# Kernel optimization log

Hardware: AMD Instinct MI355X
Metric: run time of the kernel (lower is better)

## Reference

```python
import jax, jax.numpy as jnp
import numpy as np

N_M = 100000   # metric nodes
N_A = 20000    # alert nodes
E_C = 1600000  # metric->metric 'correlation' edges
E_K = 800000   # metric->alert 'cause' edges
F_IN = 64      # raw feature dim (lazy in_channels in PyG)
DIMS = [128, 256]  # out_dim // 2**(num_layers-i-1) for lstm_dim=256, num_layers=2
NEG_SLOPE = 0.01   # nn.LeakyReLU default


def _lin(key, fan_in, fan_out):
    s = 1.0 / np.sqrt(fan_in)
    return jax.random.uniform(key, (fan_in, fan_out), minval=-s, maxval=s, dtype=jnp.float32)


def setup_inputs() -> dict:
    key = jax.random.key(0)
    ks = jax.random.split(key, 32)
    inp = {
        'x_metric': jax.random.normal(ks[0], (N_M, F_IN), dtype=jnp.float32),
        'x_alert': jax.random.normal(ks[1], (N_A, F_IN), dtype=jnp.float32),
        'w_corr': jax.random.uniform(ks[2], (E_C,), dtype=jnp.float32),
        'w_cause': jax.random.uniform(ks[3], (E_K,), dtype=jnp.float32),
        'src_corr': jax.random.randint(ks[4], (E_C,), 0, N_M, dtype=jnp.int32),
        'dst_corr': jax.random.randint(ks[5], (E_C,), 0, N_M, dtype=jnp.int32),
        'src_cause': jax.random.randint(ks[6], (E_K,), 0, N_M, dtype=jnp.int32),
        'dst_cause': jax.random.randint(ks[7], (E_K,), 0, N_A, dtype=jnp.int32),
    }
    # GraphConv params: lin_rel (with bias) applied to aggregated messages,
    # lin_root (no bias) applied to destination features. Two convs per layer.
    kidx = 8
    in_m, in_a = F_IN, F_IN
    for li, d in enumerate(DIMS):
        inp[f'Wr_c{li}'] = _lin(ks[kidx], in_m, d); kidx += 1  # corr rel
        inp[f'br_c{li}'] = jnp.zeros((d,), jnp.float32)
        inp[f'Wo_c{li}'] = _lin(ks[kidx], in_m, d); kidx += 1  # corr root (dst=metric)
        inp[f'Wr_k{li}'] = _lin(ks[kidx], in_m, d); kidx += 1  # cause rel (src=metric)
        inp[f'br_k{li}'] = jnp.zeros((d,), jnp.float32)
        inp[f'Wo_k{li}'] = _lin(ks[kidx], in_a, d); kidx += 1  # cause root (dst=alert)
        in_m, in_a = d, d
    return inp


def _leaky(x):
    return jnp.where(x > 0, x, NEG_SLOPE * x)


def reference(x_metric, x_alert, w_corr, w_cause,
              src_corr, dst_corr, src_cause, dst_cause,
              Wr_c0, br_c0, Wo_c0, Wr_k0, br_k0, Wo_k0,
              Wr_c1, br_c1, Wo_c1, Wr_k1, br_k1, Wo_k1):
    xm, xa = x_metric, x_alert
    layers = [(Wr_c0, br_c0, Wo_c0, Wr_k0, br_k0, Wo_k0),
              (Wr_c1, br_c1, Wo_c1, Wr_k1, br_k1, Wo_k1)]
    for Wrc, brc, Woc, Wrk, brk, Wok in layers:
        # metric <- metric, GraphConv aggr='add'
        msg_c = xm[src_corr] * w_corr[:, None]                 # [E_C, d_in]
        agg_c = jax.ops.segment_sum(msg_c, dst_corr, num_segments=N_M)
        new_m = agg_c @ Wrc + brc + xm @ Woc
        # alert <- metric, GraphConv aggr='max' (empty segments -> 0, torch_scatter convention)
        msg_k = xm[src_cause] * w_cause[:, None]               # [E_K, d_in]
        agg_k = jax.ops.segment_max(msg_k, dst_cause, num_segments=N_A)
        agg_k = jnp.where(jnp.isfinite(agg_k), agg_k, 0.0)
        new_a = agg_k @ Wrk + brk + xa @ Wok
        xm = _leaky(new_m)
        xa = _leaky(new_a)
    return xa  # HGNN.forward returns x['alert']
```

## Files before the change

### kernel.cpp

```cpp
#include <hip/hip_runtime.h>

#define N_M 100000
#define N_A 20000
#define E_C 1600000
#define E_K 800000
#define CH 2048
#define NXCD 8


__global__ __launch_bounds__(256) void hist_part(const int* __restrict__ dst,
                                                 int* __restrict__ deg,
                                                 int nE, int nodes_per_part) {
    int chunk = blockIdx.x >> 3, part = blockIdx.x & 7;
    int lo = part * nodes_per_part, hi = lo + nodes_per_part;
    int base = chunk * CH + threadIdx.x;
    #pragma unroll
    for (int k = 0; k < 8; ++k) {
        int e = base + k * 256;
        if (e < nE) {
            int d = dst[e];
            if (d >= lo && d < hi) atomicAdd(&deg[d], 1);
        }
    }
}

__global__ __launch_bounds__(256) void fill_eids_part(const int* __restrict__ dst,
                                                      int* __restrict__ cursor,
                                                      int* __restrict__ eids,
                                                      int nE, int nodes_per_part) {
    int chunk = blockIdx.x >> 3, part = blockIdx.x & 7;
    int lo = part * nodes_per_part, hi = lo + nodes_per_part;
    int base = chunk * CH + threadIdx.x;
    #pragma unroll
    for (int k = 0; k < 8; ++k) {
        int e = base + k * 256;
        if (e < nE) {
            int d = dst[e];
            if (d >= lo && d < hi) {
                int p = atomicAdd(&cursor[d], 1);
                eids[p] = e;
            }
        }
    }
}

__global__ __launch_bounds__(256) void fill_pay_part(const int* __restrict__ dst,
                                                     const int* __restrict__ src,
                                                     const float* __restrict__ w,
                                                     int* __restrict__ cursor,
                                                     int* __restrict__ csr_src,
                                                     float* __restrict__ csr_w,
                                                     int nE, int nodes_per_part) {
    int chunk = blockIdx.x >> 3, part = blockIdx.x & 7;
    int lo = part * nodes_per_part, hi = lo + nodes_per_part;
    int base = chunk * CH + threadIdx.x;
    #pragma unroll
    for (int k = 0; k < 8; ++k) {
        int e = base + k * 256;
        if (e < nE) {
            int d = dst[e];
            if (d >= lo && d < hi) {
                int p = atomicAdd(&cursor[d], 1);
                csr_src[p] = src[e];
                csr_w[p]   = w[e];
            }
        }
    }
}


__global__ __launch_bounds__(256) void scan_p1(const int* __restrict__ deg,
                                               int* __restrict__ partial, int n) {
    __shared__ int red[256];
    int base = blockIdx.x * CH + threadIdx.x;
    int s = 0;
    #pragma unroll
    for (int k = 0; k < 8; ++k) { int i = base + k * 256; if (i < n) s += deg[i]; }
    red[threadIdx.x] = s; __syncthreads();
    for (int off = 128; off > 0; off >>= 1) {
        if (threadIdx.x < off) red[threadIdx.x] += red[threadIdx.x + off];
        __syncthreads();
    }
    if (threadIdx.x == 0) partial[blockIdx.x] = red[0];
}

__global__ __launch_bounds__(64) void scan_p2(int* __restrict__ partial,
                                              int* __restrict__ rowptr_end, int P) {
    int lane = threadIdx.x;
    int v = (lane < P) ? partial[lane] : 0;
    int incl = v;
    for (int off = 1; off < 64; off <<= 1) {
        int t = __shfl_up(incl, off);
        if (lane >= off) incl += t;
    }
    if (lane < P) partial[lane] = incl - v;
    if (lane == 63) *rowptr_end = incl;
}

__global__ __launch_bounds__(256) void scan_p3(const int* __restrict__ deg,
                                               const int* __restrict__ partial,
                                               int* __restrict__ rowptr,
                                               int* __restrict__ cursor, int n) {
    __shared__ int buf[256];
    int base = blockIdx.x * CH;
    int v[8]; int lsum = 0;
    #pragma unroll
    for (int k = 0; k < 8; ++k) {
        int i = base + threadIdx.x * 8 + k;
        v[k] = (i < n) ? deg[i] : 0; lsum += v[k];
    }
    buf[threadIdx.x] = lsum; __syncthreads();
    for (int off = 1; off < 256; off <<= 1) {
        int t = (threadIdx.x >= off) ? buf[threadIdx.x - off] : 0;
        __syncthreads(); buf[threadIdx.x] += t; __syncthreads();
    }
    int excl = buf[threadIdx.x] - lsum + partial[blockIdx.x];
    #pragma unroll
    for (int k = 0; k < 8; ++k) {
        int i = base + threadIdx.x * 8 + k;
        if (i < n) { rowptr[i] = excl; cursor[i] = excl; }
        excl += v[k];
    }
}


__global__ __launch_bounds__(256) void agg_sum_d64(
    const float* __restrict__ x, const float* __restrict__ w, const int* __restrict__ src,
    const int* __restrict__ rowptr, const int* __restrict__ eids,
    float* __restrict__ out, int n) {
    int gw = blockIdx.x * 4 + (threadIdx.x >> 6);
    int lane = threadIdx.x & 63;
    if (gw >= n) return;
    int j = rowptr[gw], end = rowptr[gw + 1];
    float acc = 0.f;
    for (; j + 4 <= end; j += 4) {
        int e0 = eids[j], e1 = eids[j + 1], e2 = eids[j + 2], e3 = eids[j + 3];
        int s0 = src[e0], s1 = src[e1], s2 = src[e2], s3 = src[e3];
        float w0 = w[e0], w1 = w[e1], w2 = w[e2], w3 = w[e3];
        float v0 = x[(size_t)s0 * 64 + lane];
        float v1 = x[(size_t)s1 * 64 + lane];
        float v2 = x[(size_t)s2 * 64 + lane];
        float v3 = x[(size_t)s3 * 64 + lane];
        acc = fmaf(v0, w0, acc); acc = fmaf(v1, w1, acc);
        acc = fmaf(v2, w2, acc); acc = fmaf(v3, w3, acc);
    }
    for (; j < end; ++j) {
        int e = eids[j];
        acc = fmaf(x[(size_t)src[e] * 64 + lane], w[e], acc);
    }
    out[(size_t)gw * 64 + lane] = acc;
}

__global__ __launch_bounds__(256) void agg_max_d64_p(
    const float* __restrict__ x, const int* __restrict__ csr_src,
    const float* __restrict__ csr_w, const int* __restrict__ rowptr,
    float* __restrict__ out, int n) {
    int gw = blockIdx.x * 4 + (threadIdx.x >> 6);
    int lane = threadIdx.x & 63;
    if (gw >= n) return;
    int beg = rowptr[gw], end = rowptr[gw + 1];
    float acc = -INFINITY;
    int j = beg;
    for (; j + 4 <= end; j += 4) {
        int s0 = csr_src[j], s1 = csr_src[j + 1], s2 = csr_src[j + 2], s3 = csr_src[j + 3];
        float w0 = csr_w[j], w1 = csr_w[j + 1], w2 = csr_w[j + 2], w3 = csr_w[j + 3];
        float v0 = x[(size_t)s0 * 64 + lane];
        float v1 = x[(size_t)s1 * 64 + lane];
        float v2 = x[(size_t)s2 * 64 + lane];
        float v3 = x[(size_t)s3 * 64 + lane];
        acc = fmaxf(acc, v0 * w0); acc = fmaxf(acc, v1 * w1);
        acc = fmaxf(acc, v2 * w2); acc = fmaxf(acc, v3 * w3);
    }
    for (; j < end; ++j)
        acc = fmaxf(acc, x[(size_t)csr_src[j] * 64 + lane] * csr_w[j]);
    if (beg == end) acc = 0.f;
    out[(size_t)gw * 64 + lane] = acc;
}

__global__ __launch_bounds__(256) void agg_max_d128_p(
    const float* __restrict__ x, const int* __restrict__ csr_src,
    const float* __restrict__ csr_w, const int* __restrict__ rowptr,
    float* __restrict__ out, int n) {
    int gw = blockIdx.x * 4 + (threadIdx.x >> 6);
    int lane = threadIdx.x & 63;
    if (gw >= n) return;
    int beg = rowptr[gw], end = rowptr[gw + 1];
    float ax = -INFINITY, ay = -INFINITY;
    int j = beg;
    for (; j + 2 <= end; j += 2) {
        int s0 = csr_src[j], s1 = csr_src[j + 1];
        float w0 = csr_w[j], w1 = csr_w[j + 1];
        float2 v0 = ((const float2*)(x + (size_t)s0 * 128))[lane];
        float2 v1 = ((const float2*)(x + (size_t)s1 * 128))[lane];
        ax = fmaxf(ax, v0.x * w0); ay = fmaxf(ay, v0.y * w0);
        ax = fmaxf(ax, v1.x * w1); ay = fmaxf(ay, v1.y * w1);
    }
    for (; j < end; ++j) {
        float ww = csr_w[j];
        float2 v = ((const float2*)(x + (size_t)csr_src[j] * 128))[lane];
        ax = fmaxf(ax, v.x * ww); ay = fmaxf(ay, v.y * ww);
    }
    if (beg == end) { ax = 0.f; ay = 0.f; }
    ((float2*)(out + (size_t)gw * 128))[lane] = make_float2(ax, ay);
}

__global__ __launch_bounds__(256) void dual_gemm_leaky(
    const float* __restrict__ A1, const float* __restrict__ A2,
    const float* __restrict__ W1, const float* __restrict__ W2,
    const float* __restrict__ bias, float* __restrict__ out,
    int M, int N, int K1, int K2) {
    constexpr int BM = 64, BN = 64, BK = 16;
    __shared__ float sA[BK][BM];
    __shared__ float sB[BK][BN];
    const int tid = threadIdx.x;
    const int bm0 = blockIdx.y * BM;
    const int bn0 = blockIdx.x * BN;
    const int K = K1 + K2;
    float acc[4][4] = {};
    const int ty = tid >> 4, tx = tid & 15;

    for (int k0 = 0; k0 < K; k0 += BK) {
        #pragma unroll
        for (int i = 0; i < (BM * BK) / 256; ++i) {
            int idx = tid + i * 256;
            int m = idx & (BM - 1);
            int k = idx >> 6;
            int gm = bm0 + m, gk = k0 + k;
            float v = 0.0f;
            if (gm < M)
                v = (gk < K1) ? A1[(size_t)gm * K1 + gk]
                              : A2[(size_t)gm * K2 + (gk - K1)];
            sA[k][m] = v;
        }
        #pragma unroll
        for (int i = 0; i < (BK * BN) / 256; ++i) {
            int idx = tid + i * 256;
            int n = idx & (BN - 1);
            int k = idx >> 6;
            int gk = k0 + k;
            float v = (gk < K1) ? W1[(size_t)gk * N + bn0 + n]
                                : W2[(size_t)(gk - K1) * N + bn0 + n];
            sB[k][n] = v;
        }
        __syncthreads();
        #pragma unroll
        for (int kk = 0; kk < BK; ++kk) {
            float a[4], b[4];
            #pragma unroll
            for (int i = 0; i < 4; ++i) a[i] = sA[kk][ty * 4 + i];
            #pragma unroll
            for (int j = 0; j < 4; ++j) b[j] = sB[kk][tx * 4 + j];
            #pragma unroll
            for (int i = 0; i < 4; ++i)
                #pragma unroll
                for (int j = 0; j < 4; ++j)
                    acc[i][j] = fmaf(a[i], b[j], acc[i][j]);
        }
        __syncthreads();
    }
    #pragma unroll
    for (int i = 0; i < 4; ++i) {
        int gm = bm0 + ty * 4 + i;
        if (gm >= M) continue;
        #pragma unroll
        for (int j = 0; j < 4; ++j) {
            int gn = bn0 + tx * 4 + j;
            float v = acc[i][j] + bias[gn];
            out[(size_t)gm * N + gn] = (v > 0.0f) ? v : 0.01f * v;
        }
    }
}

extern "C" void kernel_launch(void* const* d_in, const int* in_sizes, int n_in,
                              void* d_out, int out_size, void* d_ws, size_t ws_size,
                              hipStream_t stream) {
    const float* x_metric = (const float*)d_in[0];
    const float* x_alert  = (const float*)d_in[1];
    const float* w_corr   = (const float*)d_in[2];
    const float* w_cause  = (const float*)d_in[3];
    const int* src_corr   = (const int*)d_in[4];
    const int* dst_corr   = (const int*)d_in[5];
    const int* src_cause  = (const int*)d_in[6];
    const int* dst_cause  = (const int*)d_in[7];
    const float* Wr_c0 = (const float*)d_in[8];
    const float* br_c0 = (const float*)d_in[9];
    const float* Wo_c0 = (const float*)d_in[10];
    const float* Wr_k0 = (const float*)d_in[11];
    const float* br_k0 = (const float*)d_in[12];
    const float* Wo_k0 = (const float*)d_in[13];
    const float* Wr_k1 = (const float*)d_in[17];
    const float* br_k1 = (const float*)d_in[18];
    const float* Wo_k1 = (const float*)d_in[19];

    float* ws = (float*)d_ws;
    float* xm0   = ws;
    float* aggk0 = ws + 11520000;
    int*   corr_rowptr = (int*)(ws + 12800000);
    int*   corr_eids   = (int*)(ws + 12900016);
    float* xa0         = ws + 12800000;
    int*   cause_rowptr = (int*)(ws + 15360000);
    int*   cause_src    = (int*)(ws + 15380016);
    float* cause_w      = ws + 16180016;
    int*   corr_cursor  = (int*)(ws + 16980016);
    int*   cause_cursor = (int*)(ws + 17080016);
    int*   corr_part    = (int*)(ws + 17100016);
    int*   cause_part   = (int*)(ws + 17100080);
    float* aggm  = ws + 17100160;
    float* aggk1 = ws + 17100160;

    const int corr_chunks  = (E_C + CH - 1) / CH;
    const int cause_chunks = (E_K + CH - 1) / CH;
    const int corr_P  = (N_M + CH - 1) / CH;
    const int cause_P = (N_A + CH - 1) / CH;

    hipMemsetAsync(corr_cursor, 0, (size_t)(N_M + N_A) * 4, stream);
    hist_part<<<corr_chunks * NXCD, 256, 0, stream>>>(dst_corr, corr_cursor, E_C, N_M / NXCD);
    hist_part<<<cause_chunks * NXCD, 256, 0, stream>>>(dst_cause, cause_cursor, E_K, N_A / NXCD);
    scan_p1<<<corr_P, 256, 0, stream>>>(corr_cursor, corr_part, N_M);
    scan_p1<<<cause_P, 256, 0, stream>>>(cause_cursor, cause_part, N_A);
    scan_p2<<<1, 64, 0, stream>>>(corr_part, corr_rowptr + N_M, corr_P);
    scan_p2<<<1, 64, 0, stream>>>(cause_part, cause_rowptr + N_A, cause_P);
    scan_p3<<<corr_P, 256, 0, stream>>>(corr_cursor, corr_part, corr_rowptr, corr_cursor, N_M);
    scan_p3<<<cause_P, 256, 0, stream>>>(cause_cursor, cause_part, cause_rowptr, cause_cursor, N_A);
    fill_eids_part<<<corr_chunks * NXCD, 256, 0, stream>>>(dst_corr, corr_cursor, corr_eids, E_C, N_M / NXCD);
    fill_pay_part<<<cause_chunks * NXCD, 256, 0, stream>>>(dst_cause, src_cause, w_cause,
                                                           cause_cursor, cause_src, cause_w,
                                                           E_K, N_A / NXCD);

    agg_sum_d64<<<(N_M + 3) / 4, 256, 0, stream>>>(x_metric, w_corr, src_corr,
                                                   corr_rowptr, corr_eids, aggm, N_M);
    agg_max_d64_p<<<(N_A + 3) / 4, 256, 0, stream>>>(x_metric, cause_src, cause_w,
                                                     cause_rowptr, aggk0, N_A);

    {
        dim3 grid(128 / 64, (N_A + 63) / 64);
        dual_gemm_leaky<<<grid, 256, 0, stream>>>(aggk0, x_alert, Wr_k0, Wo_k0, br_k0,
                                                  xa0, N_A, 128, 64, 64);
    }
    {
        dim3 grid(128 / 64, (N_M + 63) / 64);
        dual_gemm_leaky<<<grid, 256, 0, stream>>>(aggm, x_metric, Wr_c0, Wo_c0, br_c0,
                                                  xm0, N_M, 128, 64, 64);
    }

    agg_max_d128_p<<<(N_A + 3) / 4, 256, 0, stream>>>(xm0, cause_src, cause_w,
                                                      cause_rowptr, aggk1, N_A);
    {
        dim3 grid(256 / 64, (N_A + 63) / 64);
        dual_gemm_leaky<<<grid, 256, 0, stream>>>(aggk1, xa0, Wr_k1, Wo_k1, br_k1,
                                                  (float*)d_out, N_A, 256, 128, 128);
    }
}
```

Before: 719.2 us.

## Convert features and weights to bf16 and use MFMA dual GEMMs

Casts node features and weights to bf16 and stores intermediate aggregates and activations as bf16, which halves gather traffic in the aggregation kernels. The scalar FP32 dual GEMM is replaced by a templated kernel built on bf16 MFMA 16x16x32 instructions. The correlation CSR now holds src and weight payloads directly instead of edge ids, removing one level of indirection. The cost is reduced precision, which risks accuracy tolerance, plus three extra cast kernels.

```diff
diff --git a/kernel.cpp b/kernel.cpp
--- a/kernel.cpp
+++ b/kernel.cpp
@@ -7,6 +7,44 @@
 #define CH 2048
 #define NXCD 8
 
+typedef __attribute__((ext_vector_type(8)))  short  short8_t;
+typedef __attribute__((ext_vector_type(8)))  unsigned short ushort8_t;
+typedef __attribute__((ext_vector_type(4)))  unsigned short ushort4_t;
+typedef __attribute__((ext_vector_type(4)))  float  f32x4;
+
+__device__ __forceinline__ unsigned short f2b(float f) {
+    unsigned u = __float_as_uint(f);
+    return (unsigned short)((u + 0x7fffu + ((u >> 16) & 1u)) >> 16);
+}
+__device__ __forceinline__ float b2f(unsigned short h) {
+    return __uint_as_float((unsigned)h << 16);
+}
+
+__global__ __launch_bounds__(256) void cast_f32_bf16(const float* __restrict__ in,
+                                                     unsigned short* __restrict__ out, int n) {
+    int i = (blockIdx.x * 256 + threadIdx.x) * 4;
+    if (i >= n) return;
+    float4 v = *(const float4*)(in + i);
+    ushort4_t o; o.x = f2b(v.x); o.y = f2b(v.y); o.z = f2b(v.z); o.w = f2b(v.w);
+    *(ushort4_t*)(out + i) = o;
+}
+
+__global__ __launch_bounds__(256) void cast_weights(
+    const float* rc0, const float* oc0, const float* rk0, const float* ok0,
+    const float* rk1, const float* ok1, unsigned short* __restrict__ wb) {
+    int i = (blockIdx.x * 256 + threadIdx.x) * 4;
+    if (i >= 98304) return;
+    const float* src; int off;
+    if      (i < 8192)  { src = rc0; off = 0; }
+    else if (i < 16384) { src = oc0; off = 8192; }
+    else if (i < 24576) { src = rk0; off = 16384; }
+    else if (i < 32768) { src = ok0; off = 24576; }
+    else if (i < 65536) { src = rk1; off = 32768; }
+    else                { src = ok1; off = 65536; }
+    float4 v = *(const float4*)(src + (i - off));
+    ushort4_t o; o.x = f2b(v.x); o.y = f2b(v.y); o.z = f2b(v.z); o.w = f2b(v.w);
+    *(ushort4_t*)(wb + i) = o;
+}
 
 __global__ __launch_bounds__(256) void hist_part(const int* __restrict__ dst,
                                                  int* __restrict__ deg,
@@ -20,26 +58,6 @@
         if (e < nE) {
             int d = dst[e];
             if (d >= lo && d < hi) atomicAdd(&deg[d], 1);
-        }
-    }
-}
-
-__global__ __launch_bounds__(256) void fill_eids_part(const int* __restrict__ dst,
-                                                      int* __restrict__ cursor,
-                                                      int* __restrict__ eids,
-                                                      int nE, int nodes_per_part) {
-    int chunk = blockIdx.x >> 3, part = blockIdx.x & 7;
-    int lo = part * nodes_per_part, hi = lo + nodes_per_part;
-    int base = chunk * CH + threadIdx.x;
-    #pragma unroll
-    for (int k = 0; k < 8; ++k) {
-        int e = base + k * 256;
-        if (e < nE) {
-            int d = dst[e];
-            if (d >= lo && d < hi) {
-                int p = atomicAdd(&cursor[d], 1);
-                eids[p] = e;
-            }
         }
     }
 }
@@ -68,7 +86,6 @@
     }
 }
 
-
 __global__ __launch_bounds__(256) void scan_p1(const int* __restrict__ deg,
                                                int* __restrict__ partial, int n) {
     __shared__ int red[256];
@@ -123,38 +140,34 @@
     }
 }
 
-
-__global__ __launch_bounds__(256) void agg_sum_d64(
-    const float* __restrict__ x, const float* __restrict__ w, const int* __restrict__ src,
-    const int* __restrict__ rowptr, const int* __restrict__ eids,
-    float* __restrict__ out, int n) {
+__global__ __launch_bounds__(256) void agg_sum_d64_b(
+    const unsigned short* __restrict__ x, const int* __restrict__ csr_src,
+    const float* __restrict__ csr_w, const int* __restrict__ rowptr,
+    unsigned short* __restrict__ out, int n) {
     int gw = blockIdx.x * 4 + (threadIdx.x >> 6);
     int lane = threadIdx.x & 63;
     if (gw >= n) return;
     int j = rowptr[gw], end = rowptr[gw + 1];
     float acc = 0.f;
     for (; j + 4 <= end; j += 4) {
-        int e0 = eids[j], e1 = eids[j + 1], e2 = eids[j + 2], e3 = eids[j + 3];
-        int s0 = src[e0], s1 = src[e1], s2 = src[e2], s3 = src[e3];
-        float w0 = w[e0], w1 = w[e1], w2 = w[e2], w3 = w[e3];
-        float v0 = x[(size_t)s0 * 64 + lane];
-        float v1 = x[(size_t)s1 * 64 + lane];
-        float v2 = x[(size_t)s2 * 64 + lane];
-        float v3 = x[(size_t)s3 * 64 + lane];
+        int s0 = csr_src[j], s1 = csr_src[j+1], s2 = csr_src[j+2], s3 = csr_src[j+3];
+        float w0 = csr_w[j], w1 = csr_w[j+1], w2 = csr_w[j+2], w3 = csr_w[j+3];
+        float v0 = b2f(x[(size_t)s0 * 64 + lane]);
+        float v1 = b2f(x[(size_t)s1 * 64 + lane]);
+        float v2 = b2f(x[(size_t)s2 * 64 + lane]);
+        float v3 = b2f(x[(size_t)s3 * 64 + lane]);
         acc = fmaf(v0, w0, acc); acc = fmaf(v1, w1, acc);
         acc = fmaf(v2, w2, acc); acc = fmaf(v3, w3, acc);
     }
-    for (; j < end; ++j) {
-        int e = eids[j];
-        acc = fmaf(x[(size_t)src[e] * 64 + lane], w[e], acc);
-    }
-    out[(size_t)gw * 64 + lane] = acc;
-}
-
-__global__ __launch_bounds__(256) void agg_max_d64_p(
-    const float* __restrict__ x, const int* __restrict__ csr_src,
+    for (; j < end; ++j)
+        acc = fmaf(b2f(x[(size_t)csr_src[j] * 64 + lane]), csr_w[j], acc);
+    out[(size_t)gw * 64 + lane] = f2b(acc);
+}
+
+__global__ __launch_bounds__(256) void agg_max_d64_b(
+    const unsigned short* __restrict__ x, const int* __restrict__ csr_src,
     const float* __restrict__ csr_w, const int* __restrict__ rowptr,
-    float* __restrict__ out, int n) {
+    unsigned short* __restrict__ out, int n) {
     int gw = blockIdx.x * 4 + (threadIdx.x >> 6);
     int lane = threadIdx.x & 63;
     if (gw >= n) return;
@@ -162,25 +175,23 @@
     float acc = -INFINITY;
     int j = beg;
     for (; j + 4 <= end; j += 4) {
-        int s0 = csr_src[j], s1 = csr_src[j + 1], s2 = csr_src[j + 2], s3 = csr_src[j + 3];
-        float w0 = csr_w[j], w1 = csr_w[j + 1], w2 = csr_w[j + 2], w3 = csr_w[j + 3];
-        float v0 = x[(size_t)s0 * 64 + lane];
-        float v1 = x[(size_t)s1 * 64 + lane];
-        float v2 = x[(size_t)s2 * 64 + lane];
-        float v3 = x[(size_t)s3 * 64 + lane];
-        acc = fmaxf(acc, v0 * w0); acc = fmaxf(acc, v1 * w1);
-        acc = fmaxf(acc, v2 * w2); acc = fmaxf(acc, v3 * w3);
+        int s0 = csr_src[j], s1 = csr_src[j+1], s2 = csr_src[j+2], s3 = csr_src[j+3];
+        float w0 = csr_w[j], w1 = csr_w[j+1], w2 = csr_w[j+2], w3 = csr_w[j+3];
+        acc = fmaxf(acc, b2f(x[(size_t)s0 * 64 + lane]) * w0);
+        acc = fmaxf(acc, b2f(x[(size_t)s1 * 64 + lane]) * w1);
+        acc = fmaxf(acc, b2f(x[(size_t)s2 * 64 + lane]) * w2);
+        acc = fmaxf(acc, b2f(x[(size_t)s3 * 64 + lane]) * w3);
     }
     for (; j < end; ++j)
-        acc = fmaxf(acc, x[(size_t)csr_src[j] * 64 + lane] * csr_w[j]);
+        acc = fmaxf(acc, b2f(x[(size_t)csr_src[j] * 64 + lane]) * csr_w[j]);
     if (beg == end) acc = 0.f;
-    out[(size_t)gw * 64 + lane] = acc;
-}
-
-__global__ __launch_bounds__(256) void agg_max_d128_p(
-    const float* __restrict__ x, const int* __restrict__ csr_src,
+    out[(size_t)gw * 64 + lane] = f2b(acc);
+}
+
+__global__ __launch_bounds__(256) void agg_max_d128_b(
+    const unsigned short* __restrict__ x, const int* __restrict__ csr_src,
     const float* __restrict__ csr_w, const int* __restrict__ rowptr,
-    float* __restrict__ out, int n) {
+    unsigned short* __restrict__ out, int n) {
     int gw = blockIdx.x * 4 + (threadIdx.x >> 6);
     int lane = threadIdx.x & 63;
     if (gw >= n) return;
@@ -188,85 +199,103 @@
     float ax = -INFINITY, ay = -INFINITY;
     int j = beg;
     for (; j + 2 <= end; j += 2) {
-        int s0 = csr_src[j], s1 = csr_src[j + 1];
-        float w0 = csr_w[j], w1 = csr_w[j + 1];
-        float2 v0 = ((const float2*)(x + (size_t)s0 * 128))[lane];
-        float2 v1 = ((const float2*)(x + (size_t)s1 * 128))[lane];
-        ax = fmaxf(ax, v0.x * w0); ay = fmaxf(ay, v0.y * w0);
-        ax = fmaxf(ax, v1.x * w1); ay = fmaxf(ay, v1.y * w1);
+        int s0 = csr_src[j], s1 = csr_src[j+1];
+        float w0 = csr_w[j], w1 = csr_w[j+1];
+        unsigned v0 = ((const unsigned*)(x + (size_t)s0 * 128))[lane];
+        unsigned v1 = ((const unsigned*)(x + (size_t)s1 * 128))[lane];
+        ax = fmaxf(ax, b2f((unsigned short)(v0 & 0xffff)) * w0);
+        ay = fmaxf(ay, b2f((unsigned short)(v0 >> 16)) * w0);
+        ax = fmaxf(ax, b2f((unsigned short)(v1 & 0xffff)) * w1);
+        ay = fmaxf(ay, b2f((unsigned short)(v1 >> 16)) * w1);
     }
     for (; j < end; ++j) {
         float ww = csr_w[j];
-        float2 v = ((const float2*)(x + (size_t)csr_src[j] * 128))[lane];
-        ax = fmaxf(ax, v.x * ww); ay = fmaxf(ay, v.y * ww);
+        unsigned v = ((const unsigned*)(x + (size_t)csr_src[j] * 128))[lane];
+        ax = fmaxf(ax, b2f((unsigned short)(v & 0xffff)) * ww);
+        ay = fmaxf(ay, b2f((unsigned short)(v >> 16)) * ww);
     }
     if (beg == end) { ax = 0.f; ay = 0.f; }
-    ((float2*)(out + (size_t)gw * 128))[lane] = make_float2(ax, ay);
-}
-
-__global__ __launch_bounds__(256) void dual_gemm_leaky(
-    const float* __restrict__ A1, const float* __restrict__ A2,
-    const float* __restrict__ W1, const float* __restrict__ W2,
-    const float* __restrict__ bias, float* __restrict__ out,
-    int M, int N, int K1, int K2) {
-    constexpr int BM = 64, BN = 64, BK = 16;
-    __shared__ float sA[BK][BM];
-    __shared__ float sB[BK][BN];
+    ((unsigned*)(out + (size_t)gw * 128))[lane] =
+        (unsigned)f2b(ax) | ((unsigned)f2b(ay) << 16);
+}
+
+template <int K1, int K2, bool OBF>
+__global__ __launch_bounds__(256) void dual_gemm_mfma(
+    const unsigned short* __restrict__ A1, const unsigned short* __restrict__ A2,
+    const unsigned short* __restrict__ B1, const unsigned short* __restrict__ B2,
+    const float* __restrict__ bias, void* __restrict__ out, int M, int N) {
+    constexpr int KTOT = K1 + K2;
+    constexpr int LB = KTOT + 8;
+    __shared__ __align__(16) unsigned short sA[128 * 40];
+    __shared__ __align__(16) unsigned short sBT[64 * LB];
+
     const int tid = threadIdx.x;
-    const int bm0 = blockIdx.y * BM;
-    const int bn0 = blockIdx.x * BN;
-    const int K = K1 + K2;
-    float acc[4][4] = {};
-    const int ty = tid >> 4, tx = tid & 15;
-
-    for (int k0 = 0; k0 < K; k0 += BK) {
-        #pragma unroll
-        for (int i = 0; i < (BM * BK) / 256; ++i) {
-            int idx = tid + i * 256;
-            int m = idx & (BM - 1);
-            int k = idx >> 6;
-            int gm = bm0 + m, gk = k0 + k;
-            float v = 0.0f;
-            if (gm < M)
-                v = (gk < K1) ? A1[(size_t)gm * K1 + gk]
-                              : A2[(size_t)gm * K2 + (gk - K1)];
-            sA[k][m] = v;
-        }
-        #pragma unroll
-        for (int i = 0; i < (BK * BN) / 256; ++i) {
-            int idx = tid + i * 256;
-            int n = idx & (BN - 1);
-            int k = idx >> 6;
-            int gk = k0 + k;
-            float v = (gk < K1) ? W1[(size_t)gk * N + bn0 + n]
-                                : W2[(size_t)(gk - K1) * N + bn0 + n];
-            sB[k][n] = v;
-        }
+    const int lane = tid & 63, wid = tid >> 6;
+    const int wm = wid >> 1, wn = wid & 1;
+    const int bm0 = blockIdx.y * 128, n0 = blockIdx.x * 64;
+
+    for (int idx = tid; idx < KTOT * 64; idx += 256) {
+        int k = idx >> 6, n = idx & 63;
+        unsigned short v = (k < K1) ? B1[k * N + n0 + n] : B2[(k - K1) * N + n0 + n];
+        sBT[n * LB + k] = v;
+    }
+
+    f32x4 acc[4][2];
+    #pragma unroll
+    for (int i = 0; i < 4; ++i)
+        #pragma unroll
+        for (int j = 0; j < 2; ++j)
+            acc[i][j] = (f32x4){0.f, 0.f, 0.f, 0.f};
+
+    const int kk = (lane >> 4) * 8;
+    const int l15 = lane & 15;
+
+    for (int k0 = 0; k0 < KTOT; k0 += 32) {
         __syncthreads();
         #pragma unroll
-        for (int kk = 0; kk < BK; ++kk) {
-            float a[4], b[4];
+        for (int i = 0; i < 2; ++i) {
+            int v = tid + i * 256;
+            int row = v >> 2, kv = (v & 3) * 8;
+            int gm = bm0 + row, gk = k0 + kv;
+            ushort8_t val = (ushort8_t)0;
+            if (gm < M) {
+                const unsigned short* src = (gk < K1)
+                    ? (A1 + (size_t)gm * K1 + gk)
+                    : (A2 + (size_t)gm * K2 + (gk - K1));
+                val = *(const ushort8_t*)src;
+            }
+            *(ushort8_t*)(sA + row * 40 + kv) = val;
+        }
+        __syncthreads();
+
+        short8_t bfr[2];
+        #pragma unroll
+        for (int nf = 0; nf < 2; ++nf)
+            bfr[nf] = *(const short8_t*)(sBT + (wn * 32 + nf * 16 + l15) * LB + k0 + kk);
+        #pragma unroll
+        for (int mf = 0; mf < 4; ++mf) {
+            short8_t a = *(const short8_t*)(sA + (wm * 64 + mf * 16 + l15) * 40 + kk);
+            acc[mf][0] = __builtin_amdgcn_mfma_f32_16x16x32_bf16(a, bfr[0], acc[mf][0], 0, 0, 0);
+            acc[mf][1] = __builtin_amdgcn_mfma_f32_16x16x32_bf16(a, bfr[1], acc[mf][1], 0, 0, 0);
+        }
+    }
+
+    #pragma unroll
+    for (int nf = 0; nf < 2; ++nf) {
+        int col = n0 + wn * 32 + nf * 16 + l15;
+        float bcol = bias[col];
+        #pragma unroll
+        for (int mf = 0; mf < 4; ++mf) {
+            int rowb = bm0 + wm * 64 + mf * 16 + (lane >> 4) * 4;
             #pragma unroll
-            for (int i = 0; i < 4; ++i) a[i] = sA[kk][ty * 4 + i];
-            #pragma unroll
-            for (int j = 0; j < 4; ++j) b[j] = sB[kk][tx * 4 + j];
-            #pragma unroll
-            for (int i = 0; i < 4; ++i)
-                #pragma unroll
-                for (int j = 0; j < 4; ++j)
-                    acc[i][j] = fmaf(a[i], b[j], acc[i][j]);
-        }
-        __syncthreads();
-    }
-    #pragma unroll
-    for (int i = 0; i < 4; ++i) {
-        int gm = bm0 + ty * 4 + i;
-        if (gm >= M) continue;
-        #pragma unroll
-        for (int j = 0; j < 4; ++j) {
-            int gn = bn0 + tx * 4 + j;
-            float v = acc[i][j] + bias[gn];
-            out[(size_t)gm * N + gn] = (v > 0.0f) ? v : 0.01f * v;
+            for (int i = 0; i < 4; ++i) {
+                int r = rowb + i;
+                if (r >= M) continue;
+                float v = acc[mf][nf][i] + bcol;
+                v = (v > 0.f) ? v : 0.01f * v;
+                if (OBF) ((unsigned short*)out)[(size_t)r * N + col] = f2b(v);
+                else     ((float*)out)[(size_t)r * N + col] = v;
+            }
         }
     }
 }
@@ -293,25 +322,40 @@
     const float* Wo_k1 = (const float*)d_in[19];
 
     float* ws = (float*)d_ws;
-    float* xm0   = ws;
-    float* aggk0 = ws + 11520000;
-    int*   corr_rowptr = (int*)(ws + 12800000);
-    int*   corr_eids   = (int*)(ws + 12900016);
-    float* xa0         = ws + 12800000;
-    int*   cause_rowptr = (int*)(ws + 15360000);
-    int*   cause_src    = (int*)(ws + 15380016);
-    float* cause_w      = ws + 16180016;
-    int*   corr_cursor  = (int*)(ws + 16980016);
-    int*   cause_cursor = (int*)(ws + 17080016);
-    int*   corr_part    = (int*)(ws + 17100016);
-    int*   cause_part   = (int*)(ws + 17100080);
-    float* aggm  = ws + 17100160;
-    float* aggk1 = ws + 17100160;
+    unsigned short* xh_m = (unsigned short*)(ws);
+    unsigned short* xh_a = (unsigned short*)(ws + 3200000);
+    unsigned short* wb   = (unsigned short*)(ws + 3840000);
+    int*   corr_rowptr  = (int*)(ws + 3900000);
+    int*   corr_src     = (int*)(ws + 4000064);
+    float* corr_w       = (ws + 5600064);
+    int*   cause_rowptr = (int*)(ws + 7200064);
+    int*   cause_src    = (int*)(ws + 7220128);
+    float* cause_w      = (ws + 8020128);
+    int*   corr_cursor  = (int*)(ws + 8820128);
+    int*   cause_cursor = (int*)(ws + 8920128);
+    int*   corr_part    = (int*)(ws + 8940128);
+    int*   cause_part   = (int*)(ws + 8940192);
+    unsigned short* aggm  = (unsigned short*)(ws + 9000000);
+    unsigned short* aggk0 = (unsigned short*)(ws + 12200000);
+    unsigned short* xm0h  = (unsigned short*)(ws + 12840000);
+    unsigned short* xa0h  = (unsigned short*)(ws + 19240000);
+    unsigned short* aggk1 = (unsigned short*)(ws + 20520000);
+
+    const unsigned short* Wb_rc0 = wb;
+    const unsigned short* Wb_oc0 = wb + 8192;
+    const unsigned short* Wb_rk0 = wb + 16384;
+    const unsigned short* Wb_ok0 = wb + 24576;
+    const unsigned short* Wb_rk1 = wb + 32768;
+    const unsigned short* Wb_ok1 = wb + 65536;
 
     const int corr_chunks  = (E_C + CH - 1) / CH;
     const int cause_chunks = (E_K + CH - 1) / CH;
     const int corr_P  = (N_M + CH - 1) / CH;
     const int cause_P = (N_A + CH - 1) / CH;
+
+    cast_f32_bf16<<<(N_M * 64 / 4 + 255) / 256, 256, 0, stream>>>(x_metric, xh_m, N_M * 64);
+    cast_f32_bf16<<<(N_A * 64 / 4 + 255) / 256, 256, 0, stream>>>(x_alert, xh_a, N_A * 64);
+    cast_weights<<<96, 256, 0, stream>>>(Wr_c0, Wo_c0, Wr_k0, Wo_k0, Wr_k1, Wo_k1, wb);
 
     hipMemsetAsync(corr_cursor, 0, (size_t)(N_M + N_A) * 4, stream);
     hist_part<<<corr_chunks * NXCD, 256, 0, stream>>>(dst_corr, corr_cursor, E_C, N_M / NXCD);
@@ -322,32 +366,31 @@
     scan_p2<<<1, 64, 0, stream>>>(cause_part, cause_rowptr + N_A, cause_P);
     scan_p3<<<corr_P, 256, 0, stream>>>(corr_cursor, corr_part, corr_rowptr, corr_cursor, N_M);
     scan_p3<<<cause_P, 256, 0, stream>>>(cause_cursor, cause_part, cause_rowptr, cause_cursor, N_A);
-    fill_eids_part<<<corr_chunks * NXCD, 256, 0, stream>>>(dst_corr, corr_cursor, corr_eids, E_C, N_M / NXCD);
+    fill_pay_part<<<corr_chunks * NXCD, 256, 0, stream>>>(dst_corr, src_corr, w_corr,
+                                                          corr_cursor, corr_src, corr_w,
+                                                          E_C, N_M / NXCD);
     fill_pay_part<<<cause_chunks * NXCD, 256, 0, stream>>>(dst_cause, src_cause, w_cause,
                                                            cause_cursor, cause_src, cause_w,
                                                            E_K, N_A / NXCD);
 
-    agg_sum_d64<<<(N_M + 3) / 4, 256, 0, stream>>>(x_metric, w_corr, src_corr,
-                                                   corr_rowptr, corr_eids, aggm, N_M);
-    agg_max_d64_p<<<(N_A + 3) / 4, 256, 0, stream>>>(x_metric, cause_src, cause_w,
+    agg_sum_d64_b<<<(N_M + 3) / 4, 256, 0, stream>>>(xh_m, corr_src, corr_w,
+                                                     corr_rowptr, aggm, N_M);
+    agg_max_d64_b<<<(N_A + 3) / 4, 256, 0, stream>>>(xh_m, cause_src, cause_w,
                                                      cause_rowptr, aggk0, N_A);
 
-    {
-        dim3 grid(128 / 64, (N_A + 63) / 64);
-        dual_gemm_leaky<<<grid, 256, 0, stream>>>(aggk0, x_alert, Wr_k0, Wo_k0, br_k0,
-                                                  xa0, N_A, 128, 64, 64);
-    }
-    {
-        dim3 grid(128 / 64, (N_M + 63) / 64);
-        dual_gemm_leaky<<<grid, 256, 0, stream>>>(aggm, x_metric, Wr_c0, Wo_c0, br_c0,
-                                                  xm0, N_M, 128, 64, 64);
-    }
-
-    agg_max_d128_p<<<(N_A + 3) / 4, 256, 0, stream>>>(xm0, cause_src, cause_w,
+    {   dim3 grid(128 / 64, (N_A + 127) / 128);
+        dual_gemm_mfma<64, 64, true><<<grid, 256, 0, stream>>>(
+            aggk0, xh_a, Wb_rk0, Wb_ok0, br_k0, xa0h, N_A, 128);
+    }
+    {   dim3 grid(128 / 64, (N_M + 127) / 128);
+        dual_gemm_mfma<64, 64, true><<<grid, 256, 0, stream>>>(
+            aggm, xh_m, Wb_rc0, Wb_oc0, br_c0, xm0h, N_M, 128);
+    }
+
+    agg_max_d128_b<<<(N_A + 3) / 4, 256, 0, stream>>>(xm0h, cause_src, cause_w,
                                                       cause_rowptr, aggk1, N_A);
-    {
-        dim3 grid(256 / 64, (N_A + 63) / 64);
-        dual_gemm_leaky<<<grid, 256, 0, stream>>>(aggk1, xa0, Wr_k1, Wo_k1, br_k1,
-                                                  (float*)d_out, N_A, 256, 128, 128);
-    }
-}
+    {   dim3 grid(256 / 64, (N_A + 127) / 128);
+        dual_gemm_mfma<128, 128, false><<<grid, 256, 0, stream>>>(
+            aggk1, xa0h, Wb_rk1, Wb_ok1, br_k1, (float*)d_out, N_A, 256);
+    }
+}
```

After: 599.4 us. 1.2x faster.
